# Performance work log

Measured on AMD Instinct MI355X. Metric: run time of the kernel, lower is better.

The kernel has to match this reference:

```python
import jax, jax.numpy as jnp
import numpy as np

EPS = 1e-5
QMAX = 127.0

def activation_quant(x):
    # per-token (last-dim) abs-max int8 fake-quant
    x_max = jnp.clip(jnp.max(jnp.abs(x), axis=-1, keepdims=True), EPS, None)
    scale = QMAX / x_max
    q = jnp.clip(jnp.round(x * scale), -128.0, 127.0)
    return q / scale

def setup_inputs() -> dict:
    key = jax.random.key(0)
    kx, kw = jax.random.split(key)
    x = jax.random.normal(kx, (4, 8192, 2048), dtype=jnp.float32)
    # ternary {-1, 0, 1} weight, stored int8 in torch, cast to float for the GEMM
    W = jax.random.randint(kw, (2048, 2048), -1, 2).astype(jnp.float32)  # [out, in]
    return {"x": x, "W": W}

def reference(x, W):
    # straight-through estimator form: x + sg(quant(x) - x)
    x_quant = x + jax.lax.stop_gradient(activation_quant(x) - x)
    # y = x_quant @ W.T  (F.linear)
    return jnp.einsum('bsd,od->bso', x_quant, W)
```

## Files before the change

kernel.cpp:

```cpp
#include <hip/hip_runtime.h>

typedef int v4i __attribute__((ext_vector_type(4)));

#define KDIM 2048
#define NDIM 2048
#define BM 128
#define BN 128
#define BK 64

#define GLOAD_LDS16(g, l) __builtin_amdgcn_global_load_lds(                      \
    (const __attribute__((address_space(1))) void*)(g),                          \
    (__attribute__((address_space(3))) void*)(l), 16, 0, 0)

__device__ __forceinline__ int pack4q(float4 v, float s) {
  int a = __float2int_rn(v.x * s);
  int b = __float2int_rn(v.y * s);
  int c = __float2int_rn(v.z * s);
  int d = __float2int_rn(v.w * s);
  a = max(-128, min(127, a)); b = max(-128, min(127, b));
  c = max(-128, min(127, c)); d = max(-128, min(127, d));
  return (a & 0xff) | ((b & 0xff) << 8) | ((c & 0xff) << 16) | ((d & 0xff) << 24);
}

__global__ __launch_bounds__(256) void quant_rows(const float* __restrict__ x,
                                                  signed char* __restrict__ q,
                                                  float* __restrict__ rscale) {
  const int row = blockIdx.x;
  const float4* xr = (const float4*)(x + (size_t)row * KDIM);
  float4 v0 = xr[threadIdx.x];
  float4 v1 = xr[256 + threadIdx.x];
  float m = fmaxf(fmaxf(fabsf(v0.x), fabsf(v0.y)), fmaxf(fabsf(v0.z), fabsf(v0.w)));
  m = fmaxf(m, fmaxf(fmaxf(fabsf(v1.x), fabsf(v1.y)), fmaxf(fabsf(v1.z), fabsf(v1.w))));
  #pragma unroll
  for (int off = 32; off > 0; off >>= 1) m = fmaxf(m, __shfl_xor(m, off));
  __shared__ float red[4];
  if ((threadIdx.x & 63) == 0) red[threadIdx.x >> 6] = m;
  __syncthreads();
  float xmax = fmaxf(fmaxf(red[0], red[1]), fmaxf(red[2], red[3]));
  xmax = fmaxf(xmax, 1e-5f);
  const float scale = 127.0f / xmax;
  int* qr = (int*)(q + (size_t)row * KDIM);
  qr[threadIdx.x] = pack4q(v0, scale);
  qr[256 + threadIdx.x] = pack4q(v1, scale);
  if (threadIdx.x == 0) rscale[row] = xmax * (1.0f / 127.0f);
}

__global__ __launch_bounds__(256) void quant_w(const float* __restrict__ W,
                                               signed char* __restrict__ Wq) {
  const int i = blockIdx.x * 256 + threadIdx.x;
  float4 v = ((const float4*)W)[i];
  int a = (int)v.x, b = (int)v.y, c = (int)v.z, d = (int)v.w;
  ((int*)Wq)[i] = (a & 0xff) | ((b & 0xff) << 8) | ((c & 0xff) << 16) | ((d & 0xff) << 24);
}

__global__ __launch_bounds__(256) void gemm_i8(const signed char* __restrict__ A,
                                               const signed char* __restrict__ B,
                                               const float* __restrict__ rscale,
                                               float* __restrict__ C) {
  __shared__ signed char lA[BM * BK];
  __shared__ signed char lB[BN * BK];
  const int bn = blockIdx.x & (NDIM / BN - 1);
  const int bm = blockIdx.x >> 4;
  const int tid = threadIdx.x;
  const int wid = tid >> 6;
  const int lane = tid & 63;
  const int wr = wid >> 1, wc = wid & 1;

  v4i acc[4][4] = {};

  const signed char* pa = A + ((size_t)(bm * BM + wid * 32 + (lane >> 2))) * KDIM + (lane & 3) * 16;
  const signed char* pb = B + ((size_t)(bn * BN + wid * 32 + (lane >> 2))) * KDIM + (lane & 3) * 16;
  signed char* la0 = lA + wid * 2048;
  signed char* lb0 = lB + wid * 2048;

  const int ar = wr * 64 + (lane & 15);
  const int br = wc * 64 + (lane & 15);
  const int ko = (lane >> 4) * 16;

  for (int kt = 0; kt < KDIM / BK; ++kt) {
    const signed char* pak = pa + kt * BK;
    const signed char* pbk = pb + kt * BK;
    GLOAD_LDS16(pak, la0);
    GLOAD_LDS16(pak + 16 * KDIM, la0 + 1024);
    GLOAD_LDS16(pbk, lb0);
    GLOAD_LDS16(pbk + 16 * KDIM, lb0 + 1024);
    __syncthreads();

    v4i af[4], bf[4];
    #pragma unroll
    for (int m = 0; m < 4; ++m)
      af[m] = *(const v4i*)(lA + (ar + m * 16) * BK + ko);
    #pragma unroll
    for (int n = 0; n < 4; ++n)
      bf[n] = *(const v4i*)(lB + (br + n * 16) * BK + ko);

    #pragma unroll
    for (int m = 0; m < 4; ++m)
      #pragma unroll
      for (int n = 0; n < 4; ++n)
        acc[m][n] = __builtin_amdgcn_mfma_i32_16x16x64_i8(af[m], bf[n], acc[m][n], 0, 0, 0);
    __syncthreads();
  }

  const int col0 = bn * BN + wc * 64 + (lane & 15);
  const int rbase = bm * BM + wr * 64 + (lane >> 4) * 4;
  #pragma unroll
  for (int m = 0; m < 4; ++m) {
    #pragma unroll
    for (int r = 0; r < 4; ++r) {
      const int row = rbase + m * 16 + r;
      const float s = rscale[row];
      float* crow = C + (size_t)row * NDIM + col0;
      #pragma unroll
      for (int n = 0; n < 4; ++n) crow[n * 16] = (float)acc[m][n][r] * s;
    }
  }
}

extern "C" void kernel_launch(void* const* d_in, const int* in_sizes, int n_in,
                              void* d_out, int out_size, void* d_ws, size_t ws_size,
                              hipStream_t stream) {
  const float* x = (const float*)d_in[0];
  const float* W = (const float*)d_in[1];
  float* out = (float*)d_out;
  const int M = in_sizes[0] / KDIM;

  signed char* q = (signed char*)d_ws;
  signed char* Wq = q + (size_t)M * KDIM;
  float* rscale = (float*)(Wq + (size_t)NDIM * KDIM);

  quant_rows<<<M, 256, 0, stream>>>(x, q, rscale);
  quant_w<<<(NDIM * KDIM / 4) / 256, 256, 0, stream>>>(W, Wq);
  gemm_i8<<<(M / BM) * (NDIM / BN), 256, 0, stream>>>(q, Wq, rscale, out);
}
```

Measured before the change: 278.0 us.

## Rewrite int8 GEMM with 256x256 tiles, 4-stage LDS pipeline and swizzle

```diff
diff --git a/kernel.cpp b/kernel.cpp
--- a/kernel.cpp
+++ b/kernel.cpp
@@ -4,13 +4,11 @@
 
 #define KDIM 2048
 #define NDIM 2048
-#define BM 128
-#define BN 128
-#define BK 64
 
-#define GLOAD_LDS16(g, l) __builtin_amdgcn_global_load_lds(                      \
-    (const __attribute__((address_space(1))) void*)(g),                          \
+#define GLOAD16(g, l) __builtin_amdgcn_global_load_lds(                      \
+    (const __attribute__((address_space(1))) void*)(g),                      \
     (__attribute__((address_space(3))) void*)(l), 16, 0, 0)
+
 
 __device__ __forceinline__ int pack4q(float4 v, float s) {
   int a = __float2int_rn(v.x * s);
@@ -53,59 +51,115 @@
   ((int*)Wq)[i] = (a & 0xff) | ((b & 0xff) << 8) | ((c & 0xff) << 16) | ((d & 0xff) << 24);
 }
 
-__global__ __launch_bounds__(256) void gemm_i8(const signed char* __restrict__ A,
-                                               const signed char* __restrict__ B,
-                                               const float* __restrict__ rscale,
-                                               float* __restrict__ C) {
-  __shared__ signed char lA[BM * BK];
-  __shared__ signed char lB[BN * BK];
-  const int bn = blockIdx.x & (NDIM / BN - 1);
-  const int bm = blockIdx.x >> 4;
+
+#define VM8 asm volatile("s_waitcnt vmcnt(8)" ::: "memory")
+#define VM4 asm volatile("s_waitcnt vmcnt(4)" ::: "memory")
+#define VM0 asm volatile("s_waitcnt vmcnt(0)" ::: "memory")
+#define VMNONE
+
+#define STAGE_A(U, T)                                                        \
+  GLOAD16(sa + (T) * 64, lds + (U) * 32768 + dstw);                          \
+  GLOAD16(sa + (T) * 64 + 128 * KDIM, lds + (U) * 32768 + 8192 + dstw);
+#define STAGE_B(U, T)                                                        \
+  GLOAD16(sb + (T) * 64, lds + (U) * 32768 + 16384 + dstw);                  \
+  GLOAD16(sb + (T) * 64 + 128 * KDIM, lds + (U) * 32768 + 24576 + dstw);
+
+#define MF(m, n, a) acc[m][n] = __builtin_amdgcn_mfma_i32_16x16x64_i8((a), bf[n], acc[m][n], 0, 0, 0);
+
+#define KTILE(U, T, DOSTAGE, VMEND)                                          \
+  {                                                                          \
+         \
+    v4i a0 = *(const v4i*)(lds + (U) * 32768 + aRd);                         \
+    v4i a1 = *(const v4i*)(lds + (U) * 32768 + aRd + 1024);                  \
+    v4i a2 = *(const v4i*)(lds + (U) * 32768 + aRd + 2048);                  \
+    v4i a3 = *(const v4i*)(lds + (U) * 32768 + aRd + 3072);                  \
+    bf[0] = *(const v4i*)(lds + (U) * 32768 + bRd);                          \
+    bf[1] = *(const v4i*)(lds + (U) * 32768 + bRd + 1024);                   \
+    bf[2] = *(const v4i*)(lds + (U) * 32768 + bRd + 2048);                   \
+    bf[3] = *(const v4i*)(lds + (U) * 32768 + bRd + 3072);                   \
+    if (DOSTAGE) { STAGE_A((((U) + 3) & 3), (T) + 3) }                       \
+    __builtin_amdgcn_sched_barrier(0);                                       \
+    __builtin_amdgcn_s_barrier();                                            \
+    asm volatile("s_waitcnt lgkmcnt(0)" ::: "memory");                       \
+    __builtin_amdgcn_sched_barrier(0);                                       \
+    __builtin_amdgcn_s_setprio(1);                                           \
+    MF(0, 0, a0) MF(0, 1, a0) MF(0, 2, a0) MF(0, 3, a0)                      \
+    MF(1, 0, a1) MF(1, 1, a1) MF(1, 2, a1) MF(1, 3, a1)                      \
+    MF(2, 0, a2) MF(2, 1, a2) MF(2, 2, a2) MF(2, 3, a2)                      \
+    MF(3, 0, a3) MF(3, 1, a3) MF(3, 2, a3) MF(3, 3, a3)                      \
+    __builtin_amdgcn_s_setprio(0);                                           \
+    __builtin_amdgcn_sched_barrier(0);                                       \
+    __builtin_amdgcn_s_barrier();                                            \
+        \
+    v4i a4 = *(const v4i*)(lds + (U) * 32768 + aRd + 4096);                  \
+    v4i a5 = *(const v4i*)(lds + (U) * 32768 + aRd + 5120);                  \
+    v4i a6 = *(const v4i*)(lds + (U) * 32768 + aRd + 6144);                  \
+    v4i a7 = *(const v4i*)(lds + (U) * 32768 + aRd + 7168);                  \
+    if (DOSTAGE) { STAGE_B((((U) + 3) & 3), (T) + 3) }                       \
+    __builtin_amdgcn_sched_barrier(0);                                       \
+    __builtin_amdgcn_s_barrier();                                            \
+    asm volatile("s_waitcnt lgkmcnt(0)" ::: "memory");                       \
+    __builtin_amdgcn_sched_barrier(0);                                       \
+    __builtin_amdgcn_s_setprio(1);                                           \
+    MF(4, 0, a4) MF(4, 1, a4) MF(4, 2, a4) MF(4, 3, a4)                      \
+    MF(5, 0, a5) MF(5, 1, a5) MF(5, 2, a5) MF(5, 3, a5)                      \
+    MF(6, 0, a6) MF(6, 1, a6) MF(6, 2, a6) MF(6, 3, a6)                      \
+    MF(7, 0, a7) MF(7, 1, a7) MF(7, 2, a7) MF(7, 3, a7)                      \
+    __builtin_amdgcn_s_setprio(0);                                           \
+    __builtin_amdgcn_sched_barrier(0);                                       \
+    VMEND;                                                                   \
+    __builtin_amdgcn_s_barrier();                                            \
+  }
+
+__global__ __launch_bounds__(512, 2) void gemm_i8(const signed char* __restrict__ A,
+                                                  const signed char* __restrict__ B,
+                                                  const float* __restrict__ rscale,
+                                                  float* __restrict__ C) {
+  __shared__ __align__(16) signed char lds[131072];
+  const int bid = blockIdx.x;
+  const int lid = (bid & 7) * 128 + (bid >> 3);
+  const int bm = lid >> 3;
+  const int bn = lid & 7;
   const int tid = threadIdx.x;
   const int wid = tid >> 6;
   const int lane = tid & 63;
-  const int wr = wid >> 1, wc = wid & 1;
+  const int wr = wid >> 2, wc = wid & 3;
 
-  v4i acc[4][4] = {};
+  const int srow = wid * 16 + (lane >> 2);
+  const int scol = (((lane & 3) ^ ((lane >> 2) & 3)) << 4);
+  const signed char* sa = A + (size_t)(bm * 256 + srow) * KDIM + scol;
+  const signed char* sb = B + (size_t)(bn * 256 + srow) * KDIM + scol;
+  const int dstw = wid << 10;
 
-  const signed char* pa = A + ((size_t)(bm * BM + wid * 32 + (lane >> 2))) * KDIM + (lane & 3) * 16;
-  const signed char* pb = B + ((size_t)(bn * BN + wid * 32 + (lane >> 2))) * KDIM + (lane & 3) * 16;
-  signed char* la0 = lA + wid * 2048;
-  signed char* lb0 = lB + wid * 2048;
+  const int rslot = (((lane >> 4) ^ (lane & 3)) << 4);
+  const int aRd = (wr * 128 + (lane & 15)) * 64 + rslot;
+  const int bRd = 16384 + (wc * 64 + (lane & 15)) * 64 + rslot;
 
-  const int ar = wr * 64 + (lane & 15);
-  const int br = wc * 64 + (lane & 15);
-  const int ko = (lane >> 4) * 16;
+  v4i acc[8][4] = {};
+  v4i bf[4];
 
-  for (int kt = 0; kt < KDIM / BK; ++kt) {
-    const signed char* pak = pa + kt * BK;
-    const signed char* pbk = pb + kt * BK;
-    GLOAD_LDS16(pak, la0);
-    GLOAD_LDS16(pak + 16 * KDIM, la0 + 1024);
-    GLOAD_LDS16(pbk, lb0);
-    GLOAD_LDS16(pbk + 16 * KDIM, lb0 + 1024);
-    __syncthreads();
+  STAGE_A(0, 0) STAGE_B(0, 0)
+  STAGE_A(1, 1) STAGE_B(1, 1)
+  STAGE_A(2, 2) STAGE_B(2, 2)
+  VM8;
+  __builtin_amdgcn_s_barrier();
 
-    v4i af[4], bf[4];
-    #pragma unroll
-    for (int m = 0; m < 4; ++m)
-      af[m] = *(const v4i*)(lA + (ar + m * 16) * BK + ko);
-    #pragma unroll
-    for (int n = 0; n < 4; ++n)
-      bf[n] = *(const v4i*)(lB + (br + n * 16) * BK + ko);
+  for (int ti = 0; ti < 7; ++ti) {
+    const int t = ti * 4;
+    KTILE(0, t + 0, 1, VM8)
+    KTILE(1, t + 1, 1, VM8)
+    KTILE(2, t + 2, 1, VM8)
+    KTILE(3, t + 3, 1, VM8)
+  }
+  KTILE(0, 28, 1, VM8)
+  KTILE(1, 29, 0, VM4)
+  KTILE(2, 30, 0, VM0)
+  KTILE(3, 31, 0, VMNONE)
 
-    #pragma unroll
-    for (int m = 0; m < 4; ++m)
-      #pragma unroll
-      for (int n = 0; n < 4; ++n)
-        acc[m][n] = __builtin_amdgcn_mfma_i32_16x16x64_i8(af[m], bf[n], acc[m][n], 0, 0, 0);
-    __syncthreads();
-  }
-
-  const int col0 = bn * BN + wc * 64 + (lane & 15);
-  const int rbase = bm * BM + wr * 64 + (lane >> 4) * 4;
+  const int col0 = bn * 256 + wc * 64 + (lane & 15);
+  const int rbase = bm * 256 + wr * 128 + ((lane >> 4) << 2);
   #pragma unroll
-  for (int m = 0; m < 4; ++m) {
+  for (int m = 0; m < 8; ++m) {
     #pragma unroll
     for (int r = 0; r < 4; ++r) {
       const int row = rbase + m * 16 + r;
@@ -131,5 +185,5 @@
 
   quant_rows<<<M, 256, 0, stream>>>(x, q, rscale);
   quant_w<<<(NDIM * KDIM / 4) / 256, 256, 0, stream>>>(W, Wq);
-  gemm_i8<<<(M / BM) * (NDIM / BN), 256, 0, stream>>>(q, Wq, rscale, out);
+  gemm_i8<<<(M / 256) * (NDIM / 256), 512, 0, stream>>>(q, Wq, rscale, out);
 }
```

Result: faster. 239.6 us (-13.8%).

## Rewrite int8 GEMM with triple-buffered LDS pipeline, 128x256 tiles, swizzle

Applied to the files above, without the earlier changes.

```diff
diff --git a/kernel.cpp b/kernel.cpp
--- a/kernel.cpp
+++ b/kernel.cpp
@@ -4,13 +4,11 @@
 
 #define KDIM 2048
 #define NDIM 2048
-#define BM 128
-#define BN 128
-#define BK 64
 
-#define GLOAD_LDS16(g, l) __builtin_amdgcn_global_load_lds(                      \
-    (const __attribute__((address_space(1))) void*)(g),                          \
+#define GLOAD16(g, l) __builtin_amdgcn_global_load_lds(                      \
+    (const __attribute__((address_space(1))) void*)(g),                      \
     (__attribute__((address_space(3))) void*)(l), 16, 0, 0)
+
 
 __device__ __forceinline__ int pack4q(float4 v, float s) {
   int a = __float2int_rn(v.x * s);
@@ -53,57 +51,94 @@
   ((int*)Wq)[i] = (a & 0xff) | ((b & 0xff) << 8) | ((c & 0xff) << 16) | ((d & 0xff) << 24);
 }
 
-__global__ __launch_bounds__(256) void gemm_i8(const signed char* __restrict__ A,
-                                               const signed char* __restrict__ B,
-                                               const float* __restrict__ rscale,
-                                               float* __restrict__ C) {
-  __shared__ signed char lA[BM * BK];
-  __shared__ signed char lB[BN * BK];
-  const int bn = blockIdx.x & (NDIM / BN - 1);
-  const int bm = blockIdx.x >> 4;
+
+#define VM6 asm volatile("s_waitcnt vmcnt(6)" ::: "memory")
+#define VM0 asm volatile("s_waitcnt vmcnt(0)" ::: "memory")
+#define VMNONE
+
+#define STAGE(U, T)                                                          \
+  GLOAD16(sa + (T) * 64,             lds + (U) * 24576 + dstw);              \
+  GLOAD16(sa + (T) * 64 + 64 * KDIM, lds + (U) * 24576 + 4096 + dstw);       \
+  GLOAD16(sb + (T) * 64,             lds + (U) * 24576 + 8192 + dstw);       \
+  GLOAD16(sb + (T) * 64 + 64 * KDIM, lds + (U) * 24576 + 12288 + dstw);      \
+  GLOAD16(sb + (T) * 64 + 128 * KDIM, lds + (U) * 24576 + 16384 + dstw);     \
+  GLOAD16(sb + (T) * 64 + 192 * KDIM, lds + (U) * 24576 + 20480 + dstw);
+
+#define MF1(m, n, A, BF) acc[m][n] = __builtin_amdgcn_mfma_i32_16x16x64_i8((A), (BF), acc[m][n], 0, 0, 0);
+
+#define KTILE(U, T, DOSTAGE, VMEND)                                          \
+  {                                                                          \
+    if (DOSTAGE) { STAGE((((U) + 2) % 3), (T) + 2) }                         \
+    v4i b0 = *(const v4i*)(lds + (U) * 24576 + bRd);                         \
+    v4i b1 = *(const v4i*)(lds + (U) * 24576 + bRd + 1024);                  \
+    v4i b2 = *(const v4i*)(lds + (U) * 24576 + bRd + 2048);                  \
+    v4i b3 = *(const v4i*)(lds + (U) * 24576 + bRd + 3072);                  \
+    v4i b4 = *(const v4i*)(lds + (U) * 24576 + bRd + 4096);                  \
+    v4i b5 = *(const v4i*)(lds + (U) * 24576 + bRd + 5120);                  \
+    v4i b6 = *(const v4i*)(lds + (U) * 24576 + bRd + 6144);                  \
+    v4i b7 = *(const v4i*)(lds + (U) * 24576 + bRd + 7168);                  \
+    v4i a0 = *(const v4i*)(lds + (U) * 24576 + aRd);                         \
+    v4i a1 = *(const v4i*)(lds + (U) * 24576 + aRd + 1024);                  \
+    v4i a2 = *(const v4i*)(lds + (U) * 24576 + aRd + 2048);                  \
+    v4i a3 = *(const v4i*)(lds + (U) * 24576 + aRd + 3072);                  \
+    __builtin_amdgcn_s_setprio(1);                                           \
+    MF1(0, 0, a0, b0) MF1(0, 1, a0, b1) MF1(0, 2, a0, b2) MF1(0, 3, a0, b3)  \
+    MF1(0, 4, a0, b4) MF1(0, 5, a0, b5) MF1(0, 6, a0, b6) MF1(0, 7, a0, b7)  \
+    MF1(1, 0, a1, b0) MF1(1, 1, a1, b1) MF1(1, 2, a1, b2) MF1(1, 3, a1, b3)  \
+    MF1(1, 4, a1, b4) MF1(1, 5, a1, b5) MF1(1, 6, a1, b6) MF1(1, 7, a1, b7)  \
+    MF1(2, 0, a2, b0) MF1(2, 1, a2, b1) MF1(2, 2, a2, b2) MF1(2, 3, a2, b3)  \
+    MF1(2, 4, a2, b4) MF1(2, 5, a2, b5) MF1(2, 6, a2, b6) MF1(2, 7, a2, b7)  \
+    MF1(3, 0, a3, b0) MF1(3, 1, a3, b1) MF1(3, 2, a3, b2) MF1(3, 3, a3, b3)  \
+    MF1(3, 4, a3, b4) MF1(3, 5, a3, b5) MF1(3, 6, a3, b6) MF1(3, 7, a3, b7)  \
+    __builtin_amdgcn_s_setprio(0);                                           \
+    VMEND;                                                                   \
+    __builtin_amdgcn_s_barrier();                                            \
+    __builtin_amdgcn_sched_barrier(0);                                       \
+  }
+
+__global__ __launch_bounds__(256, 2) void gemm_i8(const signed char* __restrict__ A,
+                                                  const signed char* __restrict__ B,
+                                                  const float* __restrict__ rscale,
+                                                  float* __restrict__ C) {
+  __shared__ __align__(16) signed char lds[3 * 24576];
+  const int bid = blockIdx.x;
+  const int lid = (bid & 7) * 256 + (bid >> 3);
+  const int bm = lid >> 3;
+  const int bn = lid & 7;
   const int tid = threadIdx.x;
   const int wid = tid >> 6;
   const int lane = tid & 63;
   const int wr = wid >> 1, wc = wid & 1;
 
-  v4i acc[4][4] = {};
+  const int srow = wid * 16 + (lane >> 2);
+  const int scol = (((lane & 3) ^ ((lane >> 3) & 3)) << 4);
+  const signed char* sa = A + (size_t)(bm * 128 + srow) * KDIM + scol;
+  const signed char* sb = B + (size_t)(bn * 256 + srow) * KDIM + scol;
+  const int dstw = wid << 10;
 
-  const signed char* pa = A + ((size_t)(bm * BM + wid * 32 + (lane >> 2))) * KDIM + (lane & 3) * 16;
-  const signed char* pb = B + ((size_t)(bn * BN + wid * 32 + (lane >> 2))) * KDIM + (lane & 3) * 16;
-  signed char* la0 = lA + wid * 2048;
-  signed char* lb0 = lB + wid * 2048;
+  const int rslot = (((lane >> 4) ^ ((lane >> 1) & 3)) << 4);
+  const int aRd = (wr * 64 + (lane & 15)) * 64 + rslot;
+  const int bRd = 8192 + (wc * 128 + (lane & 15)) * 64 + rslot;
 
-  const int ar = wr * 64 + (lane & 15);
-  const int br = wc * 64 + (lane & 15);
-  const int ko = (lane >> 4) * 16;
+  v4i acc[4][8] = {};
 
-  for (int kt = 0; kt < KDIM / BK; ++kt) {
-    const signed char* pak = pa + kt * BK;
-    const signed char* pbk = pb + kt * BK;
-    GLOAD_LDS16(pak, la0);
-    GLOAD_LDS16(pak + 16 * KDIM, la0 + 1024);
-    GLOAD_LDS16(pbk, lb0);
-    GLOAD_LDS16(pbk + 16 * KDIM, lb0 + 1024);
-    __syncthreads();
+  STAGE(0, 0)
+  STAGE(1, 1)
+  VM6;
+  __builtin_amdgcn_s_barrier();
+  __builtin_amdgcn_sched_barrier(0);
 
-    v4i af[4], bf[4];
-    #pragma unroll
-    for (int m = 0; m < 4; ++m)
-      af[m] = *(const v4i*)(lA + (ar + m * 16) * BK + ko);
-    #pragma unroll
-    for (int n = 0; n < 4; ++n)
-      bf[n] = *(const v4i*)(lB + (br + n * 16) * BK + ko);
+  for (int ti = 0; ti < 10; ++ti) {
+    const int t = ti * 3;
+    KTILE(0, t + 0, 1, VM6)
+    KTILE(1, t + 1, 1, VM6)
+    KTILE(2, t + 2, 1, VM6)
+  }
+  KTILE(0, 30, 0, VM0)
+  KTILE(1, 31, 0, VMNONE)
 
-    #pragma unroll
-    for (int m = 0; m < 4; ++m)
-      #pragma unroll
-      for (int n = 0; n < 4; ++n)
-        acc[m][n] = __builtin_amdgcn_mfma_i32_16x16x64_i8(af[m], bf[n], acc[m][n], 0, 0, 0);
-    __syncthreads();
-  }
-
-  const int col0 = bn * BN + wc * 64 + (lane & 15);
-  const int rbase = bm * BM + wr * 64 + (lane >> 4) * 4;
+  const int col0 = bn * 256 + wc * 128 + (lane & 15);
+  const int rbase = bm * 128 + wr * 64 + ((lane >> 4) << 2);
   #pragma unroll
   for (int m = 0; m < 4; ++m) {
     #pragma unroll
@@ -112,7 +147,7 @@
       const float s = rscale[row];
       float* crow = C + (size_t)row * NDIM + col0;
       #pragma unroll
-      for (int n = 0; n < 4; ++n) crow[n * 16] = (float)acc[m][n][r] * s;
+      for (int n = 0; n < 8; ++n) crow[n * 16] = (float)acc[m][n][r] * s;
     }
   }
 }
@@ -131,5 +166,5 @@
 
   quant_rows<<<M, 256, 0, stream>>>(x, q, rscale);
   quant_w<<<(NDIM * KDIM / 4) / 256, 256, 0, stream>>>(W, Wq);
-  gemm_i8<<<(M / BM) * (NDIM / BN), 256, 0, stream>>>(q, Wq, rscale, out);
+  gemm_i8<<<(M / 128) * (NDIM / 256), 256, 0, stream>>>(q, Wq, rscale, out);
 }
```

Measured after the change: 238.1 us. 14.4% less time.
